# Performance work log

Hardware: AMD Instinct MI355X
Metric: run time of the kernel (lower is better)

Reference implementation:

```python
import jax, jax.numpy as jnp
import numpy as np

KEY_DIM = 32
VALUE_DIM = 64
HEADS = 8
CHAN = 256


def conv1x1(x, w, b):
    # x: [b, c, h, w], w: [out, c], b: [out]  (1x1 conv == channel matmul)
    return jnp.einsum('bchw,oc->bohw', x, w) + b[None, :, None, None]


def setup_inputs() -> dict:
    key = jax.random.key(0)
    ks = jax.random.split(key, 9)
    b, c, h, w = 8, CHAN, 128, 128
    qk_dim = KEY_DIM * HEADS   # 256
    v_dim = VALUE_DIM * HEADS  # 512
    s = 0.02
    return {
        'x':  jax.random.normal(ks[0], (b, c, h, w), jnp.float32),
        'Wq': jax.random.normal(ks[1], (qk_dim, c), jnp.float32) * s,
        'bq': jnp.zeros((qk_dim,), jnp.float32),
        'Wk': jax.random.normal(ks[2], (qk_dim, c), jnp.float32) * s,
        'bk': jnp.zeros((qk_dim,), jnp.float32),
        'Wv': jax.random.normal(ks[3], (v_dim, c), jnp.float32) * s,
        'bv': jnp.zeros((v_dim,), jnp.float32),
        'Wo': jax.random.normal(ks[4], (c, v_dim), jnp.float32) * s,
        'bo': jnp.zeros((c,), jnp.float32),
    }


def reference(x, Wq, bq, Wk, bk, Wv, bv, Wo, bo):
    b, c, h, w = x.shape
    n = h * w
    scale = KEY_DIM ** (-0.25)
    # 1x1 conv projections, reshape to [b, heads, d, n]
    q = conv1x1(x, Wq, bq).reshape(b, HEADS, KEY_DIM, n) * scale
    k = conv1x1(x, Wk, bk).reshape(b, HEADS, KEY_DIM, n) * scale
    v = conv1x1(x, Wv, bv).reshape(b, HEADS, VALUE_DIM, n)
    # softmax over sequence positions for keys
    k = jax.nn.softmax(k, axis=-1)
    # norm_queries=True: softmax over key dim for queries
    q = jax.nn.softmax(q, axis=-2)
    # linear attention: context [b,h,d_k,d_v], then output [b,h,d_v,n]
    ctx = jnp.einsum('bhdn,bhen->bhde', k, v)
    out = jnp.einsum('bhdn,bhde->bhen', q, ctx)
    out = out.reshape(b, HEADS * VALUE_DIM, h, w)
    return conv1x1(out, Wo, bo)
```

## Files before the change

### kernel.cpp

```cpp
#include <hip/hip_runtime.h>
#include <hip/hip_bf16.h>
#include <cstddef>


constexpr int   NPIX     = 16384;
constexpr float QK_SCALE = 0.42044820762685725f;

typedef __attribute__((ext_vector_type(8))) short          bf16x8;
typedef __attribute__((ext_vector_type(8))) unsigned short u16x8;
typedef __attribute__((ext_vector_type(4))) float          f32x4;

__device__ __forceinline__ float bf2f(unsigned short v) {
    union { unsigned int u; float f; } c; c.u = ((unsigned int)v) << 16; return c.f;
}
__device__ __forceinline__ unsigned short f2bf(float f) {
    union { __hip_bfloat16 h; unsigned short s; } c; c.h = __float2bfloat16(f); return c.s;
}

__global__ __launch_bounds__(256) void prep(
    const float* __restrict__ Wq, const float* __restrict__ Wk,
    unsigned short* __restrict__ Wqb, unsigned short* __restrict__ Wkb)
{
    const int i = blockIdx.x * 256 + threadIdx.x;
    Wqb[i] = f2bf(Wq[i]);
    Wkb[i] = f2bf(Wk[i]);
}

template<bool QPASS>
__global__ __launch_bounds__(256) void proj_mfma(
    const float* __restrict__ x, const unsigned short* __restrict__ Wb,
    const float* __restrict__ bias, unsigned short* __restrict__ eout)
{
    __shared__ alignas(16) unsigned char smem[36864];
    unsigned short (*As)[40]      = (unsigned short(*)[40])smem;
    unsigned short (*BsT)[40]     = (unsigned short(*)[40])(smem + 10240);
    unsigned short (*Cs)[64][72]  = (unsigned short(*)[64][72])smem;

    const int b  = blockIdx.z;
    const int m0 = blockIdx.y * 128;
    const int n0 = blockIdx.x * 128;
    const int t  = threadIdx.x;
    const int w  = t >> 6, l = t & 63;
    const int lm = l & 15, lg = l >> 4;
    const int mwl = (w & 1) * 64;
    const int nwl = (w >> 1) * 64;

    const float* xb = x + (size_t)b * 256 * NPIX + n0;

    const int asr = t >> 1, ash = (t & 1) * 16;
    const int np  = (t & 63) * 2, kq = (t >> 6) * 8;

    f32x4 acc[4][4] = {};
    for (int k0 = 0; k0 < 256; k0 += 32) {
        {
            const unsigned short* src = Wb + (size_t)(m0 + asr) * 256 + k0 + ash;
            *(u16x8*)&As[asr][ash]     = *(const u16x8*)src;
            *(u16x8*)&As[asr][ash + 8] = *(const u16x8*)(src + 8);
        }
        {
            const float* src = xb + (size_t)(k0 + kq) * NPIX + np;
            float2 v[8];
            #pragma unroll
            for (int r = 0; r < 8; ++r)
                v[r] = *(const float2*)(src + (size_t)r * NPIX);
            u16x8 pa, pb;
            #pragma unroll
            for (int r = 0; r < 8; ++r) { pa[r] = f2bf(v[r].x); pb[r] = f2bf(v[r].y); }
            *(u16x8*)&BsT[np][kq]     = pa;
            *(u16x8*)&BsT[np + 1][kq] = pb;
        }
        __syncthreads();
        bf16x8 afr[4], bfr[4];
        #pragma unroll
        for (int i = 0; i < 4; ++i) afr[i] = *(const bf16x8*)&As[mwl + i*16 + lm][lg*8];
        #pragma unroll
        for (int j = 0; j < 4; ++j) bfr[j] = *(const bf16x8*)&BsT[nwl + j*16 + lm][lg*8];
        #pragma unroll
        for (int i = 0; i < 4; ++i)
            #pragma unroll
            for (int j = 0; j < 4; ++j)
                acc[i][j] = __builtin_amdgcn_mfma_f32_16x16x32_bf16(afr[i], bfr[j], acc[i][j], 0, 0, 0);
        __syncthreads();
    }

    const int mw = m0 + mwl, nw = n0 + nwl;
    #pragma unroll
    for (int i = 0; i < 4; ++i) {
        const f32x4 bb4 = *(const f32x4*)(bias + mw + i*16 + lg*4);
        #pragma unroll
        for (int r = 0; r < 4; ++r) {
            const int row = i*16 + lg*4 + r;
            #pragma unroll
            for (int j = 0; j < 4; ++j) {
                const int col = j*16 + lm;
                const unsigned short bs = f2bf(__expf(QK_SCALE * (acc[i][j][r] + bb4[r])));
                if (QPASS) Cs[w][col][row] = bs;
                else       Cs[w][row][col] = bs;
            }
        }
    }
    __syncthreads();

    unsigned short* dst;
    if (QPASS) dst = eout + ((size_t)b * NPIX + nw + l) * 256 + mw;
    else       dst = eout + ((size_t)b * 256 + mw + l) * NPIX + nw;
    #pragma unroll
    for (int s8 = 0; s8 < 8; ++s8)
        *(u16x8*)(dst + s8*8) = *(const u16x8*)&Cs[w][l][s8*8];
}

__global__ __launch_bounds__(256) void ksum_pass(
    const unsigned short* __restrict__ ek, float* __restrict__ ksum)
{
    const int row = blockIdx.x;
    const unsigned short* p = ek + (size_t)row * NPIX;
    const int t = threadIdx.x;
    __shared__ float red[256];
    float s = 0.f;
    for (int i = t*8; i < NPIX; i += 2048) {
        u16x8 u = *(const u16x8*)(p + i);
        #pragma unroll
        for (int j = 0; j < 8; ++j) s += bf2f(u[j]);
    }
    red[t] = s; __syncthreads();
    for (int st = 128; st > 0; st >>= 1) {
        if (t < st) red[t] += red[t+st];
        __syncthreads();
    }
    if (t == 0) ksum[row] = red[0];
}

__global__ __launch_bounds__(256) void t_mfma(
    const unsigned short* __restrict__ ek, const float* __restrict__ x,
    float* __restrict__ Tpart)
{
    __shared__ unsigned short As[128][40];
    __shared__ unsigned short Bs[128][40];
    const int quad  = blockIdx.x;
    const int chunk = blockIdx.y;
    const int b     = blockIdx.z;
    const int mt = (quad >> 1) * 128;
    const int ct = (quad & 1) * 128;
    const int t  = threadIdx.x;
    const int w  = t >> 6, l = t & 63;
    const int lm = l & 15, lg = l >> 4;
    const int mw = (w & 1) * 64, cw = (w >> 1) * 64;
    const int sr = t >> 1, sh = (t & 1) * 16;

    const unsigned short* ekb = ek + ((size_t)b*256 + mt) * NPIX;
    const float*          xb  = x  + ((size_t)b*256 + ct) * NPIX;

    f32x4 acc[4][4] = {};
    const int p0base = chunk * 2048;
    for (int p0 = p0base; p0 < p0base + 2048; p0 += 32) {
        {
            const unsigned short* src = ekb + (size_t)sr * NPIX + p0 + sh;
            *(u16x8*)&As[sr][sh]     = *(const u16x8*)src;
            *(u16x8*)&As[sr][sh + 8] = *(const u16x8*)(src + 8);
        }
        {
            const float* src = xb + (size_t)sr * NPIX + p0 + sh;
            u16x8 a, c;
            #pragma unroll
            for (int u = 0; u < 8; ++u) { a[u] = f2bf(src[u]); c[u] = f2bf(src[8+u]); }
            *(u16x8*)&Bs[sr][sh]     = a;
            *(u16x8*)&Bs[sr][sh + 8] = c;
        }
        __syncthreads();
        bf16x8 afr[4], bfr[4];
        #pragma unroll
        for (int i = 0; i < 4; ++i) afr[i] = *(const bf16x8*)&As[mw + i*16 + lm][lg*8];
        #pragma unroll
        for (int j = 0; j < 4; ++j) bfr[j] = *(const bf16x8*)&Bs[cw + j*16 + lm][lg*8];
        #pragma unroll
        for (int i = 0; i < 4; ++i)
            #pragma unroll
            for (int j = 0; j < 4; ++j)
                acc[i][j] = __builtin_amdgcn_mfma_f32_16x16x32_bf16(afr[i], bfr[j], acc[i][j], 0, 0, 0);
        __syncthreads();
    }

    float* dst = Tpart + (((size_t)b*8 + chunk) * 256) * 256;
    #pragma unroll
    for (int i = 0; i < 4; ++i)
        #pragma unroll
        for (int r = 0; r < 4; ++r) {
            const int gm = mt + mw + i*16 + lg*4 + r;
            #pragma unroll
            for (int j = 0; j < 4; ++j)
                dst[(size_t)gm * 256 + ct + cw + j*16 + lm] = acc[i][j][r];
        }
}

__global__ __launch_bounds__(256) void treduce(
    float* __restrict__ Tpart, const float* __restrict__ ksum)
{
    const int gid = blockIdx.x * 256 + threadIdx.x;
    const int b   = gid >> 14;
    const int rem = gid & 16383;
    const int r   = rem >> 6;
    const int c4  = (rem & 63) * 4;
    float* base = Tpart + (((size_t)b*8) * 256 + r) * 256 + c4;
    f32x4 s = *(f32x4*)base;
    #pragma unroll
    for (int ch = 1; ch < 8; ++ch) {
        f32x4 v = *(const f32x4*)(base + (size_t)ch * 65536);
        s.x += v.x; s.y += v.y; s.z += v.z; s.w += v.w;
    }
    const float inv = 1.0f / ksum[b*256 + r];
    s.x *= inv; s.y *= inv; s.z *= inv; s.w *= inv;
    *(f32x4*)base = s;
}

__global__ __launch_bounds__(256) void ctx_pass(
    const float* __restrict__ Tpart, const float* __restrict__ Wv,
    const float* __restrict__ bv, float* __restrict__ ctx)
{
    const int gid = blockIdx.x * 256 + threadIdx.x;
    const int b   = gid >> 14;
    const int rem = gid & 16383;
    const int h   = rem >> 11;
    const int de  = rem & 2047;
    const int d   = de >> 6;
    const int e   = de & 63;
    const float* tp = Tpart + (((size_t)b*8) * 256 + h*32 + d) * 256;
    const float* wv = Wv + (size_t)(h*64 + e) * 256;
    float sx = 0.f, sy = 0.f, sz = 0.f, sw = 0.f;
    #pragma unroll 8
    for (int c = 0; c < 256; c += 4) {
        f32x4 a = *(const f32x4*)(tp + c);
        f32x4 w = *(const f32x4*)(wv + c);
        sx = fmaf(a.x, w.x, sx); sy = fmaf(a.y, w.y, sy);
        sz = fmaf(a.z, w.z, sz); sw = fmaf(a.w, w.w, sw);
    }
    ctx[gid] = (sx + sy) + (sz + sw) + bv[h*64 + e];
}

__global__ __launch_bounds__(256) void mpass(
    const float* __restrict__ ctx, const float* __restrict__ Wo,
    unsigned short* __restrict__ Mb)
{
    const int gid = blockIdx.x * 256 + threadIdx.x;
    const int b   = gid >> 16;
    const int rem = gid & 65535;
    const int o   = rem >> 8;
    const int dg  = rem & 255;
    const int h   = dg >> 5;
    const int d   = dg & 31;
    const float* cp = ctx + ((size_t)b*8 + h) * 2048 + d*64;
    const float* wp = Wo + (size_t)o * 512 + h*64;
    float sx = 0.f, sy = 0.f, sz = 0.f, sw = 0.f;
    #pragma unroll
    for (int e = 0; e < 64; e += 4) {
        f32x4 a = *(const f32x4*)(cp + e);
        f32x4 w = *(const f32x4*)(wp + e);
        sx = fmaf(a.x, w.x, sx); sy = fmaf(a.y, w.y, sy);
        sz = fmaf(a.z, w.z, sz); sw = fmaf(a.w, w.w, sw);
    }
    Mb[((size_t)b*256 + o) * 256 + dg] = f2bf((sx + sy) + (sz + sw));
}

__global__ __launch_bounds__(256) void invz_pass(
    const unsigned short* __restrict__ eqT, float* __restrict__ invZ)
{
    const int b = blockIdx.y;
    const int n = blockIdx.x * 256 + threadIdx.x;
    const unsigned short* row = eqT + ((size_t)b * NPIX + n) * 256;
    float* o = invZ + ((size_t)b * NPIX + n) * 8;
    #pragma unroll
    for (int h = 0; h < 8; ++h) {
        float s = 0.f;
        #pragma unroll
        for (int u = 0; u < 4; ++u) {
            u16x8 v = *(const u16x8*)(row + h*32 + u*8);
            #pragma unroll
            for (int e = 0; e < 8; ++e) s += bf2f(v[e]);
        }
        o[h] = 1.0f / s;
    }
}

__global__ __launch_bounds__(256) void out_mfma(
    const unsigned short* __restrict__ eqT, const float* __restrict__ invZ,
    const unsigned short* __restrict__ Mb, const float* __restrict__ bo,
    float* __restrict__ out)
{
    __shared__ unsigned short As[128][40];
    __shared__ unsigned short Bs[128][40];
    const int b  = blockIdx.z;
    const int m0 = blockIdx.y * 128;
    const int n0 = blockIdx.x * 128;
    const int t  = threadIdx.x;
    const int w  = t >> 6, l = t & 63;
    const int lm = l & 15, lg = l >> 4;
    const int mw = (w & 1) * 64, nw = (w >> 1) * 64;
    const int sr = t >> 1, sh = (t & 1) * 16;

    const unsigned short* Ab  = Mb  + ((size_t)b*256 + m0) * 256;
    const unsigned short* Bb  = eqT + (size_t)b * NPIX * 256;
    const float*          izb = invZ + (size_t)b * NPIX * 8;

    f32x4 acc[4][4] = {};
    for (int k0 = 0; k0 < 256; k0 += 32) {
        {
            const unsigned short* src = Ab + (size_t)sr * 256 + k0 + sh;
            *(u16x8*)&As[sr][sh]     = *(const u16x8*)src;
            *(u16x8*)&As[sr][sh + 8] = *(const u16x8*)(src + 8);
        }
        {
            const unsigned short* src = Bb + (size_t)(n0 + sr) * 256 + k0 + sh;
            const float iz = izb[(size_t)(n0 + sr) * 8 + (k0 >> 5)];
            u16x8 a = *(const u16x8*)src, c = *(const u16x8*)(src + 8);
            u16x8 oa, oc;
            #pragma unroll
            for (int u = 0; u < 8; ++u) {
                oa[u] = f2bf(bf2f(a[u]) * iz);
                oc[u] = f2bf(bf2f(c[u]) * iz);
            }
            *(u16x8*)&Bs[sr][sh]     = oa;
            *(u16x8*)&Bs[sr][sh + 8] = oc;
        }
        __syncthreads();
        bf16x8 afr[4], bfr[4];
        #pragma unroll
        for (int i = 0; i < 4; ++i) afr[i] = *(const bf16x8*)&As[mw + i*16 + lm][lg*8];
        #pragma unroll
        for (int j = 0; j < 4; ++j) bfr[j] = *(const bf16x8*)&Bs[nw + j*16 + lm][lg*8];
        #pragma unroll
        for (int i = 0; i < 4; ++i)
            #pragma unroll
            for (int j = 0; j < 4; ++j)
                acc[i][j] = __builtin_amdgcn_mfma_f32_16x16x32_bf16(afr[i], bfr[j], acc[i][j], 0, 0, 0);
        __syncthreads();
    }

    #pragma unroll
    for (int i = 0; i < 4; ++i) {
        const f32x4 bb4 = *(const f32x4*)(bo + m0 + mw + i*16 + lg*4);
        #pragma unroll
        for (int r = 0; r < 4; ++r) {
            const int gm = m0 + mw + i*16 + lg*4 + r;
            float* dst = out + ((size_t)b*256 + gm) * NPIX + n0 + nw;
            #pragma unroll
            for (int j = 0; j < 4; ++j)
                dst[j*16 + lm] = acc[i][j][r] + bb4[r];
        }
    }
}

extern "C" void kernel_launch(void* const* d_in, const int* in_sizes, int n_in,
                              void* d_out, int out_size, void* d_ws, size_t ws_size,
                              hipStream_t stream)
{
    const float* x  = (const float*)d_in[0];
    const float* Wq = (const float*)d_in[1];
    const float* bq = (const float*)d_in[2];
    const float* Wk = (const float*)d_in[3];
    const float* bk = (const float*)d_in[4];
    const float* Wv = (const float*)d_in[5];
    const float* bv = (const float*)d_in[6];
    const float* Wo = (const float*)d_in[7];
    const float* bo = (const float*)d_in[8];
    float* out = (float*)d_out;

    if (ws_size < (size_t)89399296) return;
    char* wsb = (char*)d_ws;
    unsigned short* ekq  = (unsigned short*)wsb;
    float*          Tpart= (float*)(wsb + 67108864);
    float*          invZ = (float*)(wsb + 83886080);
    float*          ksum = (float*)(wsb + 88080384);
    unsigned short* Mb   = (unsigned short*)(wsb + 88088576);
    unsigned short* Wqb  = (unsigned short*)(wsb + 89137152);
    unsigned short* Wkb  = (unsigned short*)(wsb + 89268224);
    float*          ctx  = invZ;

    prep             <<<256,              256, 0, stream>>>(Wq, Wk, Wqb, Wkb);
    proj_mfma<false> <<<dim3(128, 2, 8),  256, 0, stream>>>(x, Wkb, bk, ekq);
    ksum_pass        <<<2048,             256, 0, stream>>>(ekq, ksum);
    t_mfma           <<<dim3(4, 8, 8),    256, 0, stream>>>(ekq, x, Tpart);
    treduce          <<<512,              256, 0, stream>>>(Tpart, ksum);
    ctx_pass         <<<512,              256, 0, stream>>>(Tpart, Wv, bv, ctx);
    mpass            <<<2048,             256, 0, stream>>>(ctx, Wo, Mb);
    proj_mfma<true>  <<<dim3(128, 2, 8),  256, 0, stream>>>(x, Wqb, bq, ekq);
    invz_pass        <<<dim3(64, 8),      256, 0, stream>>>(ekq, invZ);
    out_mfma         <<<dim3(128, 2, 8),  256, 0, stream>>>(ekq, invZ, Mb, bo, out);
}
```

Before: 309.3 us.

## Fuse key sum into T GEMM, keep q channel-major, load weights directly

The separate ksum_pass kernel is removed. Per-row key sums are accumulated inside t_mfma from the already-loaded exp(k) tiles and reduced across chunks in treduce. The q projection now writes channel-major like k, so the shared-memory transpose epilogue goes away, and invz_pass and out_mfma read that layout. Weight (A) fragments are read straight from global memory instead of being staged through LDS. The trade-off is uncoalesced 2-byte epilogue stores, strided loads in invz_pass, and uncached global A loads inside the k-loop.

Result: slower. 340.1 us (+9.9%).

```diff
diff --git a/kernel.cpp b/kernel.cpp
--- a/kernel.cpp
+++ b/kernel.cpp
@@ -26,16 +26,11 @@
     Wkb[i] = f2bf(Wk[i]);
 }
 
-template<bool QPASS>
 __global__ __launch_bounds__(256) void proj_mfma(
     const float* __restrict__ x, const unsigned short* __restrict__ Wb,
     const float* __restrict__ bias, unsigned short* __restrict__ eout)
 {
-    __shared__ alignas(16) unsigned char smem[36864];
-    unsigned short (*As)[40]      = (unsigned short(*)[40])smem;
-    unsigned short (*BsT)[40]     = (unsigned short(*)[40])(smem + 10240);
-    unsigned short (*Cs)[64][72]  = (unsigned short(*)[64][72])smem;
-
+    __shared__ unsigned short BsT[128][40];
     const int b  = blockIdx.z;
     const int m0 = blockIdx.y * 128;
     const int n0 = blockIdx.x * 128;
@@ -46,18 +41,13 @@
     const int nwl = (w >> 1) * 64;
 
     const float* xb = x + (size_t)b * 256 * NPIX + n0;
-
-    const int asr = t >> 1, ash = (t & 1) * 16;
-    const int np  = (t & 63) * 2, kq = (t >> 6) * 8;
+    const unsigned short* arow = Wb + (size_t)(m0 + mwl) * 256;
+
+    const int np = (t & 63) * 2, kq = (t >> 6) * 8;
 
     f32x4 acc[4][4] = {};
     for (int k0 = 0; k0 < 256; k0 += 32) {
         {
-            const unsigned short* src = Wb + (size_t)(m0 + asr) * 256 + k0 + ash;
-            *(u16x8*)&As[asr][ash]     = *(const u16x8*)src;
-            *(u16x8*)&As[asr][ash + 8] = *(const u16x8*)(src + 8);
-        }
-        {
             const float* src = xb + (size_t)(k0 + kq) * NPIX + np;
             float2 v[8];
             #pragma unroll
@@ -72,7 +62,8 @@
         __syncthreads();
         bf16x8 afr[4], bfr[4];
         #pragma unroll
-        for (int i = 0; i < 4; ++i) afr[i] = *(const bf16x8*)&As[mwl + i*16 + lm][lg*8];
+        for (int i = 0; i < 4; ++i)
+            afr[i] = *(const bf16x8*)(arow + (size_t)(i*16 + lm) * 256 + k0 + lg*8);
         #pragma unroll
         for (int j = 0; j < 4; ++j) bfr[j] = *(const bf16x8*)&BsT[nwl + j*16 + lm][lg*8];
         #pragma unroll
@@ -89,50 +80,18 @@
         const f32x4 bb4 = *(const f32x4*)(bias + mw + i*16 + lg*4);
         #pragma unroll
         for (int r = 0; r < 4; ++r) {
-            const int row = i*16 + lg*4 + r;
-            #pragma unroll
-            for (int j = 0; j < 4; ++j) {
-                const int col = j*16 + lm;
-                const unsigned short bs = f2bf(__expf(QK_SCALE * (acc[i][j][r] + bb4[r])));
-                if (QPASS) Cs[w][col][row] = bs;
-                else       Cs[w][row][col] = bs;
-            }
-        }
-    }
-    __syncthreads();
-
-    unsigned short* dst;
-    if (QPASS) dst = eout + ((size_t)b * NPIX + nw + l) * 256 + mw;
-    else       dst = eout + ((size_t)b * 256 + mw + l) * NPIX + nw;
-    #pragma unroll
-    for (int s8 = 0; s8 < 8; ++s8)
-        *(u16x8*)(dst + s8*8) = *(const u16x8*)&Cs[w][l][s8*8];
-}
-
-__global__ __launch_bounds__(256) void ksum_pass(
-    const unsigned short* __restrict__ ek, float* __restrict__ ksum)
-{
-    const int row = blockIdx.x;
-    const unsigned short* p = ek + (size_t)row * NPIX;
-    const int t = threadIdx.x;
-    __shared__ float red[256];
-    float s = 0.f;
-    for (int i = t*8; i < NPIX; i += 2048) {
-        u16x8 u = *(const u16x8*)(p + i);
-        #pragma unroll
-        for (int j = 0; j < 8; ++j) s += bf2f(u[j]);
-    }
-    red[t] = s; __syncthreads();
-    for (int st = 128; st > 0; st >>= 1) {
-        if (t < st) red[t] += red[t+st];
-        __syncthreads();
-    }
-    if (t == 0) ksum[row] = red[0];
+            const int gm = mw + i*16 + lg*4 + r;
+            unsigned short* dst = eout + ((size_t)b*256 + gm) * NPIX + nw;
+            #pragma unroll
+            for (int j = 0; j < 4; ++j)
+                dst[j*16 + lm] = f2bf(__expf(QK_SCALE * (acc[i][j][r] + bb4[r])));
+        }
+    }
 }
 
 __global__ __launch_bounds__(256) void t_mfma(
     const unsigned short* __restrict__ ek, const float* __restrict__ x,
-    float* __restrict__ Tpart)
+    float* __restrict__ Tpart, float* __restrict__ ksump)
 {
     __shared__ unsigned short As[128][40];
     __shared__ unsigned short Bs[128][40];
@@ -141,6 +100,7 @@
     const int b     = blockIdx.z;
     const int mt = (quad >> 1) * 128;
     const int ct = (quad & 1) * 128;
+    const bool do_ks = (quad & 1) == 0;
     const int t  = threadIdx.x;
     const int w  = t >> 6, l = t & 63;
     const int lm = l & 15, lg = l >> 4;
@@ -151,12 +111,19 @@
     const float*          xb  = x  + ((size_t)b*256 + ct) * NPIX;
 
     f32x4 acc[4][4] = {};
+    float krow = 0.f;
     const int p0base = chunk * 2048;
     for (int p0 = p0base; p0 < p0base + 2048; p0 += 32) {
         {
             const unsigned short* src = ekb + (size_t)sr * NPIX + p0 + sh;
-            *(u16x8*)&As[sr][sh]     = *(const u16x8*)src;
-            *(u16x8*)&As[sr][sh + 8] = *(const u16x8*)(src + 8);
+            u16x8 a0 = *(const u16x8*)src;
+            u16x8 a1 = *(const u16x8*)(src + 8);
+            *(u16x8*)&As[sr][sh]     = a0;
+            *(u16x8*)&As[sr][sh + 8] = a1;
+            if (do_ks) {
+                #pragma unroll
+                for (int u = 0; u < 8; ++u) krow += bf2f(a0[u]) + bf2f(a1[u]);
+            }
         }
         {
             const float* src = xb + (size_t)sr * NPIX + p0 + sh;
@@ -180,6 +147,12 @@
         __syncthreads();
     }
 
+    if (do_ks) {
+        krow += __shfl_xor(krow, 1, 64);
+        if ((t & 1) == 0)
+            ksump[((size_t)b*8 + chunk)*256 + mt + sr] = krow;
+    }
+
     float* dst = Tpart + (((size_t)b*8 + chunk) * 256) * 256;
     #pragma unroll
     for (int i = 0; i < 4; ++i)
@@ -193,13 +166,16 @@
 }
 
 __global__ __launch_bounds__(256) void treduce(
-    float* __restrict__ Tpart, const float* __restrict__ ksum)
+    float* __restrict__ Tpart, const float* __restrict__ ksump)
 {
     const int gid = blockIdx.x * 256 + threadIdx.x;
     const int b   = gid >> 14;
     const int rem = gid & 16383;
     const int r   = rem >> 6;
     const int c4  = (rem & 63) * 4;
+    float ks = 0.f;
+    #pragma unroll
+    for (int ch = 0; ch < 8; ++ch) ks += ksump[((size_t)b*8 + ch)*256 + r];
     float* base = Tpart + (((size_t)b*8) * 256 + r) * 256 + c4;
     f32x4 s = *(f32x4*)base;
     #pragma unroll
@@ -207,7 +183,7 @@
         f32x4 v = *(const f32x4*)(base + (size_t)ch * 65536);
         s.x += v.x; s.y += v.y; s.z += v.z; s.w += v.w;
     }
-    const float inv = 1.0f / ksum[b*256 + r];
+    const float inv = 1.0f / ks;
     s.x *= inv; s.y *= inv; s.z *= inv; s.w *= inv;
     *(f32x4*)base = s;
 }
@@ -261,32 +237,28 @@
 }
 
 __global__ __launch_bounds__(256) void invz_pass(
-    const unsigned short* __restrict__ eqT, float* __restrict__ invZ)
+    const unsigned short* __restrict__ eq, float* __restrict__ invZ)
 {
     const int b = blockIdx.y;
     const int n = blockIdx.x * 256 + threadIdx.x;
-    const unsigned short* row = eqT + ((size_t)b * NPIX + n) * 256;
+    const unsigned short* base = eq + (size_t)b * 256 * NPIX + n;
     float* o = invZ + ((size_t)b * NPIX + n) * 8;
     #pragma unroll
     for (int h = 0; h < 8; ++h) {
         float s = 0.f;
         #pragma unroll
-        for (int u = 0; u < 4; ++u) {
-            u16x8 v = *(const u16x8*)(row + h*32 + u*8);
-            #pragma unroll
-            for (int e = 0; e < 8; ++e) s += bf2f(v[e]);
-        }
+        for (int d = 0; d < 32; ++d)
+            s += bf2f(base[(size_t)(h*32 + d) * NPIX]);
         o[h] = 1.0f / s;
     }
 }
 
 __global__ __launch_bounds__(256) void out_mfma(
-    const unsigned short* __restrict__ eqT, const float* __restrict__ invZ,
+    const unsigned short* __restrict__ eq, const float* __restrict__ invZ,
     const unsigned short* __restrict__ Mb, const float* __restrict__ bo,
     float* __restrict__ out)
 {
-    __shared__ unsigned short As[128][40];
-    __shared__ unsigned short Bs[128][40];
+    __shared__ unsigned short BsT[128][40];
     const int b  = blockIdx.z;
     const int m0 = blockIdx.y * 128;
     const int n0 = blockIdx.x * 128;
@@ -294,38 +266,39 @@
     const int w  = t >> 6, l = t & 63;
     const int lm = l & 15, lg = l >> 4;
     const int mw = (w & 1) * 64, nw = (w >> 1) * 64;
-    const int sr = t >> 1, sh = (t & 1) * 16;
-
-    const unsigned short* Ab  = Mb  + ((size_t)b*256 + m0) * 256;
-    const unsigned short* Bb  = eqT + (size_t)b * NPIX * 256;
-    const float*          izb = invZ + (size_t)b * NPIX * 8;
+    const int np = (t & 63) * 2, kq = (t >> 6) * 8;
+
+    const unsigned short* Ab  = Mb + ((size_t)b*256 + m0 + mw) * 256;
+    const unsigned short* Bb  = eq + (size_t)b * 256 * NPIX + n0;
+    const float*          izb = invZ + ((size_t)b * NPIX + n0) * 8;
 
     f32x4 acc[4][4] = {};
     for (int k0 = 0; k0 < 256; k0 += 32) {
+        const int h = k0 >> 5;
         {
-            const unsigned short* src = Ab + (size_t)sr * 256 + k0 + sh;
-            *(u16x8*)&As[sr][sh]     = *(const u16x8*)src;
-            *(u16x8*)&As[sr][sh + 8] = *(const u16x8*)(src + 8);
-        }
-        {
-            const unsigned short* src = Bb + (size_t)(n0 + sr) * 256 + k0 + sh;
-            const float iz = izb[(size_t)(n0 + sr) * 8 + (k0 >> 5)];
-            u16x8 a = *(const u16x8*)src, c = *(const u16x8*)(src + 8);
-            u16x8 oa, oc;
-            #pragma unroll
-            for (int u = 0; u < 8; ++u) {
-                oa[u] = f2bf(bf2f(a[u]) * iz);
-                oc[u] = f2bf(bf2f(c[u]) * iz);
+            const unsigned short* src = Bb + (size_t)(k0 + kq) * NPIX + np;
+            const float iz0 = izb[(size_t)np * 8 + h];
+            const float iz1 = izb[(size_t)(np + 1) * 8 + h];
+            ushort2 v[8];
+            #pragma unroll
+            for (int r = 0; r < 8; ++r)
+                v[r] = *(const ushort2*)(src + (size_t)r * NPIX);
+            u16x8 pa, pb;
+            #pragma unroll
+            for (int r = 0; r < 8; ++r) {
+                pa[r] = f2bf(bf2f(v[r].x) * iz0);
+                pb[r] = f2bf(bf2f(v[r].y) * iz1);
             }
-            *(u16x8*)&Bs[sr][sh]     = oa;
-            *(u16x8*)&Bs[sr][sh + 8] = oc;
+            *(u16x8*)&BsT[np][kq]     = pa;
+            *(u16x8*)&BsT[np + 1][kq] = pb;
         }
         __syncthreads();
         bf16x8 afr[4], bfr[4];
         #pragma unroll
-        for (int i = 0; i < 4; ++i) afr[i] = *(const bf16x8*)&As[mw + i*16 + lm][lg*8];
-        #pragma unroll
-        for (int j = 0; j < 4; ++j) bfr[j] = *(const bf16x8*)&Bs[nw + j*16 + lm][lg*8];
+        for (int i = 0; i < 4; ++i)
+            afr[i] = *(const bf16x8*)(Ab + (size_t)(i*16 + lm) * 256 + k0 + lg*8);
+        #pragma unroll
+        for (int j = 0; j < 4; ++j) bfr[j] = *(const bf16x8*)&BsT[nw + j*16 + lm][lg*8];
         #pragma unroll
         for (int i = 0; i < 4; ++i)
             #pragma unroll
@@ -368,20 +341,19 @@
     unsigned short* ekq  = (unsigned short*)wsb;
     float*          Tpart= (float*)(wsb + 67108864);
     float*          invZ = (float*)(wsb + 83886080);
-    float*          ksum = (float*)(wsb + 88080384);
+    float*          ctx  = (float*)(wsb + 83886080);
+    float*          ksump= (float*)(wsb + 83886080 + 1048576);
     unsigned short* Mb   = (unsigned short*)(wsb + 88088576);
     unsigned short* Wqb  = (unsigned short*)(wsb + 89137152);
     unsigned short* Wkb  = (unsigned short*)(wsb + 89268224);
-    float*          ctx  = invZ;
-
-    prep             <<<256,              256, 0, stream>>>(Wq, Wk, Wqb, Wkb);
-    proj_mfma<false> <<<dim3(128, 2, 8),  256, 0, stream>>>(x, Wkb, bk, ekq);
-    ksum_pass        <<<2048,             256, 0, stream>>>(ekq, ksum);
-    t_mfma           <<<dim3(4, 8, 8),    256, 0, stream>>>(ekq, x, Tpart);
-    treduce          <<<512,              256, 0, stream>>>(Tpart, ksum);
-    ctx_pass         <<<512,              256, 0, stream>>>(Tpart, Wv, bv, ctx);
-    mpass            <<<2048,             256, 0, stream>>>(ctx, Wo, Mb);
-    proj_mfma<true>  <<<dim3(128, 2, 8),  256, 0, stream>>>(x, Wqb, bq, ekq);
-    invz_pass        <<<dim3(64, 8),      256, 0, stream>>>(ekq, invZ);
-    out_mfma         <<<dim3(128, 2, 8),  256, 0, stream>>>(ekq, invZ, Mb, bo, out);
-}
+
+    prep      <<<256,             256, 0, stream>>>(Wq, Wk, Wqb, Wkb);
+    proj_mfma <<<dim3(128, 2, 8), 256, 0, stream>>>(x, Wkb, bk, ekq);
+    t_mfma    <<<dim3(4, 8, 8),   256, 0, stream>>>(ekq, x, Tpart, ksump);
+    treduce   <<<512,             256, 0, stream>>>(Tpart, ksump);
+    ctx_pass  <<<512,             256, 0, stream>>>(Tpart, Wv, bv, ctx);
+    mpass     <<<2048,            256, 0, stream>>>(ctx, Wo, Mb);
+    proj_mfma <<<dim3(128, 2, 8), 256, 0, stream>>>(x, Wqb, bq, ekq);
+    invz_pass <<<dim3(64, 8),     256, 0, stream>>>(ekq, invZ);
+    out_mfma  <<<dim3(128, 2, 8), 256, 0, stream>>>(ekq, invZ, Mb, bo, out);
+}
```
